# Performance work log

Hardware: AMD Instinct MI355X
Metric: run time of the kernel (lower is better)

## Reference

```python
import jax, jax.numpy as jnp
import numpy as np


def setup_inputs() -> dict:
    key = jax.random.key(0)
    k1, k2 = jax.random.split(key, 2)
    N, C, H, W, G = 64, 256, 56, 56, 32
    x = jax.random.normal(k1, (N, C, H, W), dtype=jnp.float32)
    # fc: Linear(batch_size*2 -> group)
    fc_w = jax.random.normal(k2, (G, 2 * N), dtype=jnp.float32) * 0.05
    fc_b = jnp.zeros((G,), dtype=jnp.float32)
    # affine params (1, C, 1, 1), init ones/zeros as in the module
    weight = jnp.ones((1, C, 1, 1), dtype=jnp.float32)
    bias = jnp.zeros((1, C, 1, 1), dtype=jnp.float32)
    return {"x": x, "fc_w": fc_w, "fc_b": fc_b, "weight": weight, "bias": bias, "group": G}


def reference(x, fc_w, fc_b, weight, bias, group):
    eps = 1e-5
    N, C, H, W = x.shape
    hw = H * W
    # --- routing features: per-channel mean/var over (N is kept, reduce HW) ---
    # torch: x_ = x.transpose(0,1).view(C,N,HW); mean/var(-1) with unbiased var (ddof=1)
    mean_cn = jnp.mean(x, axis=(2, 3)).T           # [C, N]
    var_cn = jnp.var(x, axis=(2, 3), ddof=1).T     # [C, N]
    s = jnp.concatenate([mean_cn, var_cn], axis=1)  # [C, 2N]
    probs = jax.nn.softmax(s @ fc_w.T + fc_b, axis=1)  # [C, G]
    g = jnp.argmax(probs, axis=1)                  # [C] channel -> group
    onehot = jax.nn.one_hot(g, group, dtype=x.dtype)  # [C, G]
    # --- per-(sample, group) mean/var via segment reduce expressed as GEMM ---
    s1 = jnp.sum(x, axis=(2, 3))        # [N, C]
    s2 = jnp.sum(x * x, axis=(2, 3))    # [N, C]
    S1 = s1 @ onehot                    # [N, G]
    S2 = s2 @ onehot                    # [N, G]
    cnt = jnp.sum(onehot, axis=0) * hw  # [G] elements per (n, g)
    mean_g = S1 / jnp.maximum(cnt, 1.0)                          # [N, G]
    # unbiased variance (torch .var default): (sum_sq - n*mean^2)/(n-1)
    var_g = (S2 - S1 * mean_g) / jnp.maximum(cnt - 1.0, 1.0)     # [N, G]
    # empty groups are skipped in the original; no channel maps to them, so
    # the guarded denominators only prevent NaNs and never affect outputs.
    mean_c = mean_g[:, g]  # [N, C] gather per-channel stats
    var_c = var_g[:, g]    # [N, C]
    xn = (x - mean_c[:, :, None, None]) * jax.lax.rsqrt(var_c + eps)[:, :, None, None]
    return xn * weight + bias
```

## Files before the change

kernel.cpp:

```cpp
#include <hip/hip_runtime.h>

constexpr int N_  = 64;
constexpr int C_  = 256;
constexpr int HW_ = 56 * 56;
constexpr int G_  = 32;
constexpr int NC_ = N_ * C_;
constexpr float EPS_ = 1e-5f;

typedef float f32x4 __attribute__((ext_vector_type(4)));

__global__ __launch_bounds__(256) void k_sums(const float* __restrict__ x,
                                              float* __restrict__ s1,
                                              float* __restrict__ s2) {
    const int wave = threadIdx.x >> 6;
    const int lane = threadIdx.x & 63;
    const int nc = blockIdx.x * 4 + wave;
    const f32x4* xp = reinterpret_cast<const f32x4*>(x + (size_t)nc * HW_);
    f32x4 v[12];
    #pragma unroll
    for (int k = 0; k < 12; ++k) v[k] = xp[lane + k * 64];
    f32x4 vt;
    const bool tail = lane < 16;
    if (tail) vt = xp[768 + lane];
    float a = 0.f, b = 0.f;
    #pragma unroll
    for (int k = 0; k < 12; ++k) {
        a += (v[k].x + v[k].y) + (v[k].z + v[k].w);
        b += (v[k].x * v[k].x + v[k].y * v[k].y) + (v[k].z * v[k].z + v[k].w * v[k].w);
    }
    if (tail) {
        a += (vt.x + vt.y) + (vt.z + vt.w);
        b += (vt.x * vt.x + vt.y * vt.y) + (vt.z * vt.z + vt.w * vt.w);
    }
    #pragma unroll
    for (int off = 32; off; off >>= 1) {
        a += __shfl_down(a, off, 64);
        b += __shfl_down(b, off, 64);
    }
    if (lane == 0) { s1[nc] = a; s2[nc] = b; }
}

__global__ __launch_bounds__(64) void k_logits(const float* __restrict__ s1,
                                               const float* __restrict__ s2,
                                               const float* __restrict__ fc_w,
                                               const float* __restrict__ fc_b,
                                               int* __restrict__ gidx) {
    const int c = blockIdx.x;
    const int t = threadIdx.x;
    const int g = t & 31, half = t >> 5;
    const float inv_hw  = 1.f / (float)HW_;
    const float inv_hw1 = 1.f / (float)(HW_ - 1);
    const float* wg = fc_w + g * (2 * N_);
    float acc = half ? 0.f : fc_b[g];
    const int n0 = half * 32;
    #pragma unroll 8
    for (int n = n0; n < n0 + 32; ++n) {
        const float v1 = s1[n * C_ + c];
        const float v2 = s2[n * C_ + c];
        const float m  = v1 * inv_hw;
        const float vr = (v2 - v1 * m) * inv_hw1;
        acc += m * wg[n] + vr * wg[N_ + n];
    }
    acc += __shfl_down(acc, 32, 64);
    __shared__ float lg[G_];
    if (half == 0) lg[g] = acc;
    __syncthreads();
    if (t == 0) {
        float best = lg[0];
        int bi = 0;
        for (int g2 = 1; g2 < G_; ++g2) {
            const float v = lg[g2];
            if (v > best) { best = v; bi = g2; }
        }
        gidx[c] = bi;
    }
}

__global__ __launch_bounds__(256) void k_group(const float* __restrict__ s1,
                                               const float* __restrict__ s2,
                                               const int* __restrict__ gidx,
                                               const float* __restrict__ weight,
                                               const float* __restrict__ bias,
                                               float* __restrict__ scale,
                                               float* __restrict__ shift) {
    const int n = blockIdx.x;
    const int c = threadIdx.x;
    __shared__ float r1[C_], r2[C_];
    __shared__ int   gi[C_];
    __shared__ float mg[G_], ig[G_];
    r1[c] = s1[n * C_ + c];
    r2[c] = s2[n * C_ + c];
    gi[c] = gidx[c];
    __syncthreads();
    if (c < G_) {
        float A = 0.f, B = 0.f;
        int k = 0;
        for (int cc = 0; cc < C_; ++cc) {
            if (gi[cc] == c) { A += r1[cc]; B += r2[cc]; ++k; }
        }
        const float cf = (float)k * (float)HW_;
        const float m  = A / fmaxf(cf, 1.f);
        const float vr = (B - A * m) / fmaxf(cf - 1.f, 1.f);
        mg[c] = m;
        ig[c] = rsqrtf(vr + EPS_);
    }
    __syncthreads();
    const int g = gi[c];
    const float sc = ig[g] * weight[c];
    scale[n * C_ + c] = sc;
    shift[n * C_ + c] = bias[c] - mg[g] * sc;
}

__global__ __launch_bounds__(256) void k_norm(const float* __restrict__ x,
                                              const float* __restrict__ scale,
                                              const float* __restrict__ shift,
                                              float* __restrict__ out) {
    const int wave = threadIdx.x >> 6;
    const int lane = threadIdx.x & 63;
    const int nc = blockIdx.x * 4 + wave;
    const float sc = scale[nc];
    const float sh = shift[nc];
    const f32x4* xp = reinterpret_cast<const f32x4*>(x + (size_t)nc * HW_);
    f32x4* op = reinterpret_cast<f32x4*>(out + (size_t)nc * HW_);
    f32x4 v[12];
    #pragma unroll
    for (int k = 0; k < 12; ++k) v[k] = xp[lane + k * 64];
    f32x4 vt;
    const bool tail = lane < 16;
    if (tail) vt = xp[768 + lane];
    #pragma unroll
    for (int k = 0; k < 12; ++k) {
        v[k] = v[k] * sc + sh;
        __builtin_nontemporal_store(v[k], op + lane + k * 64);
    }
    if (tail) {
        vt = vt * sc + sh;
        __builtin_nontemporal_store(vt, op + 768 + lane);
    }
}

extern "C" void kernel_launch(void* const* d_in, const int* in_sizes, int n_in,
                              void* d_out, int out_size, void* d_ws, size_t ws_size,
                              hipStream_t stream) {
    const float* x      = (const float*)d_in[0];
    const float* fc_w   = (const float*)d_in[1];
    const float* fc_b   = (const float*)d_in[2];
    const float* weight = (const float*)d_in[3];
    const float* bias   = (const float*)d_in[4];
    float* out = (float*)d_out;

    float* ws    = (float*)d_ws;
    float* s1    = ws;
    float* s2    = ws + NC_;
    float* scale = ws + 2 * NC_;
    float* shift = ws + 3 * NC_;
    int*   gidx  = (int*)(ws + 4 * NC_);

    k_sums  <<<NC_ / 4, 256, 0, stream>>>(x, s1, s2);
    k_logits<<<C_,       64, 0, stream>>>(s1, s2, fc_w, fc_b, gidx);
    k_group <<<N_,      256, 0, stream>>>(s1, s2, gidx, weight, bias, scale, shift);
    k_norm  <<<NC_ / 4, 256, 0, stream>>>(x, scale, shift, out);
}
```

Before: 120.6 us.

## Fuse four kernels into one cooperative kernel keeping part of x in registers

Replaces the four-kernel pipeline (sums, logits, group stats, normalize) with a single cooperative kernel of 256 blocks that uses grid-wide syncs between phases. Each wave holds the first 5 of 12 vector chunks of its 8 channel slices in registers across the syncs, so the normalize pass reloads only the rest of x instead of all of it. This cuts launch overhead and some re-reading of x from memory. The cost is two grid barriers, heavy register pressure that may limit occupancy or spill, and only 256 blocks to hide memory latency.

```diff
diff --git a/kernel.cpp b/kernel.cpp
--- a/kernel.cpp
+++ b/kernel.cpp
@@ -1,141 +1,168 @@
 #include <hip/hip_runtime.h>
+#include <hip/hip_cooperative_groups.h>
+
+namespace cg = cooperative_groups;
 
 constexpr int N_  = 64;
 constexpr int C_  = 256;
 constexpr int HW_ = 56 * 56;
+constexpr int NV_ = HW_ / 4;
 constexpr int G_  = 32;
 constexpr int NC_ = N_ * C_;
 constexpr float EPS_ = 1e-5f;
 
 typedef float f32x4 __attribute__((ext_vector_type(4)));
 
-__global__ __launch_bounds__(256) void k_sums(const float* __restrict__ x,
-                                              float* __restrict__ s1,
-                                              float* __restrict__ s2) {
-    const int wave = threadIdx.x >> 6;
-    const int lane = threadIdx.x & 63;
-    const int nc = blockIdx.x * 4 + wave;
-    const f32x4* xp = reinterpret_cast<const f32x4*>(x + (size_t)nc * HW_);
-    f32x4 v[12];
+__global__ __launch_bounds__(512, 2) void k_fused(
+    const float* __restrict__ x,
+    const float* __restrict__ fc_w,
+    const float* __restrict__ fc_b,
+    const float* __restrict__ weight,
+    const float* __restrict__ bias,
+    float* __restrict__ out,
+    float* __restrict__ s1,
+    float* __restrict__ s2,
+    int*   __restrict__ gidxg)
+{
+    const int b    = blockIdx.x;
+    const int t    = threadIdx.x;
+    const int w    = t >> 6;
+    const int lane = t & 63;
+    const int n    = b >> 2;
+    const int c0   = (b & 3) * 64;
+    const int slice0 = b * 64 + w * 8;
+
+    __shared__ float r1s[C_], r2s[C_];
+    __shared__ int   gidxL[C_];
+    __shared__ float mgs[G_], igs[G_];
+    __shared__ float scs[64], shs[64];
+
+    f32x4 keep[8][5];
     #pragma unroll
-    for (int k = 0; k < 12; ++k) v[k] = xp[lane + k * 64];
-    f32x4 vt;
-    const bool tail = lane < 16;
-    if (tail) vt = xp[768 + lane];
-    float a = 0.f, b = 0.f;
-    #pragma unroll
-    for (int k = 0; k < 12; ++k) {
-        a += (v[k].x + v[k].y) + (v[k].z + v[k].w);
-        b += (v[k].x * v[k].x + v[k].y * v[k].y) + (v[k].z * v[k].z + v[k].w * v[k].w);
+    for (int s = 0; s < 8; ++s) {
+        const int nc = slice0 + s;
+        const f32x4* xp = reinterpret_cast<const f32x4*>(x) + (size_t)nc * NV_;
+        #pragma unroll
+        for (int k = 0; k < 5; ++k) keep[s][k] = xp[lane + k * 64];
+        f32x4 v5  = xp[lane + 320];
+        f32x4 v6  = xp[lane + 384];
+        f32x4 v7  = xp[lane + 448];
+        f32x4 v8  = xp[lane + 512];
+        f32x4 v9  = xp[lane + 576];
+        f32x4 v10 = xp[lane + 640];
+        f32x4 v11 = xp[lane + 704];
+        const bool tail = lane < 16;
+        f32x4 vt;
+        if (tail) vt = xp[768 + lane];
+        float a = 0.f, q = 0.f;
+        #pragma unroll
+        for (int k = 0; k < 5; ++k) {
+            f32x4 v = keep[s][k];
+            a += (v.x + v.y) + (v.z + v.w);
+            q += (v.x * v.x + v.y * v.y) + (v.z * v.z + v.w * v.w);
+        }
+        a += (v5.x + v5.y) + (v5.z + v5.w);   q += (v5.x*v5.x + v5.y*v5.y) + (v5.z*v5.z + v5.w*v5.w);
+        a += (v6.x + v6.y) + (v6.z + v6.w);   q += (v6.x*v6.x + v6.y*v6.y) + (v6.z*v6.z + v6.w*v6.w);
+        a += (v7.x + v7.y) + (v7.z + v7.w);   q += (v7.x*v7.x + v7.y*v7.y) + (v7.z*v7.z + v7.w*v7.w);
+        a += (v8.x + v8.y) + (v8.z + v8.w);   q += (v8.x*v8.x + v8.y*v8.y) + (v8.z*v8.z + v8.w*v8.w);
+        a += (v9.x + v9.y) + (v9.z + v9.w);   q += (v9.x*v9.x + v9.y*v9.y) + (v9.z*v9.z + v9.w*v9.w);
+        a += (v10.x + v10.y) + (v10.z + v10.w); q += (v10.x*v10.x + v10.y*v10.y) + (v10.z*v10.z + v10.w*v10.w);
+        a += (v11.x + v11.y) + (v11.z + v11.w); q += (v11.x*v11.x + v11.y*v11.y) + (v11.z*v11.z + v11.w*v11.w);
+        if (tail) {
+            a += (vt.x + vt.y) + (vt.z + vt.w);
+            q += (vt.x*vt.x + vt.y*vt.y) + (vt.z*vt.z + vt.w*vt.w);
+        }
+        #pragma unroll
+        for (int off = 32; off; off >>= 1) {
+            a += __shfl_down(a, off, 64);
+            q += __shfl_down(q, off, 64);
+        }
+        if (lane == 0) {
+            __hip_atomic_store(&s1[nc], a, __ATOMIC_RELAXED, __HIP_MEMORY_SCOPE_AGENT);
+            __hip_atomic_store(&s2[nc], q, __ATOMIC_RELAXED, __HIP_MEMORY_SCOPE_AGENT);
+        }
     }
-    if (tail) {
-        a += (vt.x + vt.y) + (vt.z + vt.w);
-        b += (vt.x * vt.x + vt.y * vt.y) + (vt.z * vt.z + vt.w * vt.w);
+
+    __threadfence();
+    cg::this_grid().sync();
+
+    if (t < 64) {
+        const int c = b;
+        const int g = lane & 31, half = lane >> 5;
+        const float inv_hw  = 1.f / (float)HW_;
+        const float inv_hw1 = 1.f / (float)(HW_ - 1);
+        const float* wg = fc_w + g * (2 * N_);
+        float acc = half ? 0.f : fc_b[g];
+        const int n0 = half * 32;
+        #pragma unroll
+        for (int nn = n0; nn < n0 + 32; ++nn) {
+            const float a1 = __hip_atomic_load(&s1[nn * C_ + c], __ATOMIC_RELAXED, __HIP_MEMORY_SCOPE_AGENT);
+            const float a2 = __hip_atomic_load(&s2[nn * C_ + c], __ATOMIC_RELAXED, __HIP_MEMORY_SCOPE_AGENT);
+            const float m  = a1 * inv_hw;
+            const float vr = (a2 - a1 * m) * inv_hw1;
+            acc += m * wg[nn] + vr * wg[N_ + nn];
+        }
+        acc += __shfl_down(acc, 32, 64);
+        float bv = acc; int bi = g;
+        #pragma unroll
+        for (int off = 16; off; off >>= 1) {
+            float ov = __shfl_down(bv, off, 32);
+            int   oi = __shfl_down(bi, off, 32);
+            if (ov > bv || (ov == bv && oi < bi)) { bv = ov; bi = oi; }
+        }
+        if (lane == 0)
+            __hip_atomic_store(&gidxg[c], bi, __ATOMIC_RELAXED, __HIP_MEMORY_SCOPE_AGENT);
     }
-    #pragma unroll
-    for (int off = 32; off; off >>= 1) {
-        a += __shfl_down(a, off, 64);
-        b += __shfl_down(b, off, 64);
+
+    __threadfence();
+    cg::this_grid().sync();
+
+    if (t < 256) {
+        r1s[t]   = __hip_atomic_load(&s1[n * C_ + t], __ATOMIC_RELAXED, __HIP_MEMORY_SCOPE_AGENT);
+        gidxL[t] = __hip_atomic_load(&gidxg[t],       __ATOMIC_RELAXED, __HIP_MEMORY_SCOPE_AGENT);
+    } else {
+        r2s[t - 256] = __hip_atomic_load(&s2[n * C_ + (t - 256)], __ATOMIC_RELAXED, __HIP_MEMORY_SCOPE_AGENT);
     }
-    if (lane == 0) { s1[nc] = a; s2[nc] = b; }
-}
-
-__global__ __launch_bounds__(64) void k_logits(const float* __restrict__ s1,
-                                               const float* __restrict__ s2,
-                                               const float* __restrict__ fc_w,
-                                               const float* __restrict__ fc_b,
-                                               int* __restrict__ gidx) {
-    const int c = blockIdx.x;
-    const int t = threadIdx.x;
-    const int g = t & 31, half = t >> 5;
-    const float inv_hw  = 1.f / (float)HW_;
-    const float inv_hw1 = 1.f / (float)(HW_ - 1);
-    const float* wg = fc_w + g * (2 * N_);
-    float acc = half ? 0.f : fc_b[g];
-    const int n0 = half * 32;
-    #pragma unroll 8
-    for (int n = n0; n < n0 + 32; ++n) {
-        const float v1 = s1[n * C_ + c];
-        const float v2 = s2[n * C_ + c];
-        const float m  = v1 * inv_hw;
-        const float vr = (v2 - v1 * m) * inv_hw1;
-        acc += m * wg[n] + vr * wg[N_ + n];
-    }
-    acc += __shfl_down(acc, 32, 64);
-    __shared__ float lg[G_];
-    if (half == 0) lg[g] = acc;
     __syncthreads();
-    if (t == 0) {
-        float best = lg[0];
-        int bi = 0;
-        for (int g2 = 1; g2 < G_; ++g2) {
-            const float v = lg[g2];
-            if (v > best) { best = v; bi = g2; }
-        }
-        gidx[c] = bi;
-    }
-}
-
-__global__ __launch_bounds__(256) void k_group(const float* __restrict__ s1,
-                                               const float* __restrict__ s2,
-                                               const int* __restrict__ gidx,
-                                               const float* __restrict__ weight,
-                                               const float* __restrict__ bias,
-                                               float* __restrict__ scale,
-                                               float* __restrict__ shift) {
-    const int n = blockIdx.x;
-    const int c = threadIdx.x;
-    __shared__ float r1[C_], r2[C_];
-    __shared__ int   gi[C_];
-    __shared__ float mg[G_], ig[G_];
-    r1[c] = s1[n * C_ + c];
-    r2[c] = s2[n * C_ + c];
-    gi[c] = gidx[c];
-    __syncthreads();
-    if (c < G_) {
-        float A = 0.f, B = 0.f;
-        int k = 0;
-        for (int cc = 0; cc < C_; ++cc) {
-            if (gi[cc] == c) { A += r1[cc]; B += r2[cc]; ++k; }
-        }
+    if (t < G_) {
+        float A = 0.f, B = 0.f; int k = 0;
+        for (int cc = 0; cc < C_; ++cc)
+            if (gidxL[cc] == t) { A += r1s[cc]; B += r2s[cc]; ++k; }
         const float cf = (float)k * (float)HW_;
         const float m  = A / fmaxf(cf, 1.f);
         const float vr = (B - A * m) / fmaxf(cf - 1.f, 1.f);
-        mg[c] = m;
-        ig[c] = rsqrtf(vr + EPS_);
+        mgs[t] = m;
+        igs[t] = rsqrtf(vr + EPS_);
     }
     __syncthreads();
-    const int g = gi[c];
-    const float sc = ig[g] * weight[c];
-    scale[n * C_ + c] = sc;
-    shift[n * C_ + c] = bias[c] - mg[g] * sc;
-}
+    if (t < 64) {
+        const int c = c0 + t;
+        const int g = gidxL[c];
+        const float sc = igs[g] * weight[c];
+        scs[t] = sc;
+        shs[t] = bias[c] - mgs[g] * sc;
+    }
+    __syncthreads();
 
-__global__ __launch_bounds__(256) void k_norm(const float* __restrict__ x,
-                                              const float* __restrict__ scale,
-                                              const float* __restrict__ shift,
-                                              float* __restrict__ out) {
-    const int wave = threadIdx.x >> 6;
-    const int lane = threadIdx.x & 63;
-    const int nc = blockIdx.x * 4 + wave;
-    const float sc = scale[nc];
-    const float sh = shift[nc];
-    const f32x4* xp = reinterpret_cast<const f32x4*>(x + (size_t)nc * HW_);
-    f32x4* op = reinterpret_cast<f32x4*>(out + (size_t)nc * HW_);
-    f32x4 v[12];
     #pragma unroll
-    for (int k = 0; k < 12; ++k) v[k] = xp[lane + k * 64];
-    f32x4 vt;
-    const bool tail = lane < 16;
-    if (tail) vt = xp[768 + lane];
-    #pragma unroll
-    for (int k = 0; k < 12; ++k) {
-        v[k] = v[k] * sc + sh;
-        __builtin_nontemporal_store(v[k], op + lane + k * 64);
-    }
-    if (tail) {
-        vt = vt * sc + sh;
-        __builtin_nontemporal_store(vt, op + 768 + lane);
+    for (int s = 0; s < 8; ++s) {
+        const int nc = slice0 + s;
+        const float sc = scs[w * 8 + s];
+        const float sh = shs[w * 8 + s];
+        const f32x4* xp = reinterpret_cast<const f32x4*>(x)   + (size_t)nc * NV_;
+        f32x4*       op = reinterpret_cast<f32x4*>(out)       + (size_t)nc * NV_;
+        #pragma unroll
+        for (int k = 0; k < 5; ++k)
+            __builtin_nontemporal_store(keep[s][k] * sc + sh, op + lane + k * 64);
+        #pragma unroll
+        for (int k = 5; k < 12; ++k) {
+            f32x4 v = xp[lane + k * 64];
+            __builtin_nontemporal_store(v * sc + sh, op + lane + k * 64);
+        }
+        if (lane < 16) {
+            f32x4 v = xp[768 + lane];
+            __builtin_nontemporal_store(v * sc + sh, op + 768 + lane);
+        }
     }
 }
 
@@ -147,17 +174,14 @@
     const float* fc_b   = (const float*)d_in[2];
     const float* weight = (const float*)d_in[3];
     const float* bias   = (const float*)d_in[4];
-    float* out = (float*)d_out;
+    float* outp = (float*)d_out;
 
-    float* ws    = (float*)d_ws;
-    float* s1    = ws;
-    float* s2    = ws + NC_;
-    float* scale = ws + 2 * NC_;
-    float* shift = ws + 3 * NC_;
-    int*   gidx  = (int*)(ws + 4 * NC_);
+    float* ws = (float*)d_ws;
+    float* s1 = ws;
+    float* s2 = ws + NC_;
+    int*   gidxg = (int*)(ws + 2 * NC_);
 
-    k_sums  <<<NC_ / 4, 256, 0, stream>>>(x, s1, s2);
-    k_logits<<<C_,       64, 0, stream>>>(s1, s2, fc_w, fc_b, gidx);
-    k_group <<<N_,      256, 0, stream>>>(s1, s2, gidx, weight, bias, scale, shift);
-    k_norm  <<<NC_ / 4, 256, 0, stream>>>(x, scale, shift, out);
+    void* args[] = { (void*)&x, (void*)&fc_w, (void*)&fc_b, (void*)&weight, (void*)&bias,
+                     (void*)&outp, (void*)&s1, (void*)&s2, (void*)&gidxg };
+    hipLaunchCooperativeKernel((void*)k_fused, dim3(256), dim3(512), args, 0, stream);
 }
```

Result: slower. 289.3 us (+139.8%).

## Fuse four-stage pipeline into one cooperative persistent kernel with grid syncs

Applied to the files above, without the earlier changes.

Replaces the four separate launches (sums, logits, group stats, normalize) with a single cooperative persistent kernel that separates the phases with grid-wide syncs, falling back to the old launches if occupancy is too low. The aim is to remove launch gaps and tail effects between the small middle kernels. In exchange it adds three grid barriers, limits the grid to 1024 blocks, and leaves the x reads in the normalize phase still going through memory, since 205 MB of x cannot stay cached. The logits argmax now uses a wave shuffle reduction instead of a serial loop.

```diff
diff --git a/kernel.cpp b/kernel.cpp
--- a/kernel.cpp
+++ b/kernel.cpp
@@ -1,13 +1,151 @@
 #include <hip/hip_runtime.h>
+#include <hip/hip_cooperative_groups.h>
+
+namespace cg = cooperative_groups;
 
 constexpr int N_  = 64;
 constexpr int C_  = 256;
 constexpr int HW_ = 56 * 56;
+constexpr int NV_ = HW_ / 4;
 constexpr int G_  = 32;
 constexpr int NC_ = N_ * C_;
 constexpr float EPS_ = 1e-5f;
 
 typedef float f32x4 __attribute__((ext_vector_type(4)));
+
+__global__ __launch_bounds__(256, 4) void k_fused(
+    const float* __restrict__ x,
+    const float* __restrict__ fc_w,
+    const float* __restrict__ fc_b,
+    const float* __restrict__ weight,
+    const float* __restrict__ bias,
+    float* __restrict__ out,
+    float* __restrict__ s1,
+    float* __restrict__ s2,
+    float* __restrict__ scale,
+    float* __restrict__ shift,
+    int*   __restrict__ gidxg)
+{
+    const int t    = threadIdx.x;
+    const int w    = t >> 6;
+    const int lane = t & 63;
+    const int nwaves = gridDim.x * 4;
+
+    __shared__ float r1s[C_], r2s[C_];
+    __shared__ int   gidxL[C_];
+    __shared__ float mgs[G_], igs[G_];
+
+    for (int nc = blockIdx.x * 4 + w; nc < NC_; nc += nwaves) {
+        const f32x4* xp = reinterpret_cast<const f32x4*>(x) + (size_t)nc * NV_;
+        f32x4 v[12];
+        #pragma unroll
+        for (int k = 0; k < 12; ++k) v[k] = xp[lane + k * 64];
+        const bool tail = lane < 16;
+        f32x4 vt;
+        if (tail) vt = xp[768 + lane];
+        float a = 0.f, q = 0.f;
+        #pragma unroll
+        for (int k = 0; k < 12; ++k) {
+            a += (v[k].x + v[k].y) + (v[k].z + v[k].w);
+            q += (v[k].x * v[k].x + v[k].y * v[k].y) + (v[k].z * v[k].z + v[k].w * v[k].w);
+        }
+        if (tail) {
+            a += (vt.x + vt.y) + (vt.z + vt.w);
+            q += (vt.x * vt.x + vt.y * vt.y) + (vt.z * vt.z + vt.w * vt.w);
+        }
+        #pragma unroll
+        for (int off = 32; off; off >>= 1) {
+            a += __shfl_down(a, off, 64);
+            q += __shfl_down(q, off, 64);
+        }
+        if (lane == 0) {
+            __hip_atomic_store(&s1[nc], a, __ATOMIC_RELAXED, __HIP_MEMORY_SCOPE_AGENT);
+            __hip_atomic_store(&s2[nc], q, __ATOMIC_RELAXED, __HIP_MEMORY_SCOPE_AGENT);
+        }
+    }
+
+    __threadfence();
+    cg::this_grid().sync();
+
+    for (int c = blockIdx.x; c < C_; c += gridDim.x) {
+        if (t < 64) {
+            const int g = lane & 31, half = lane >> 5;
+            const float inv_hw  = 1.f / (float)HW_;
+            const float inv_hw1 = 1.f / (float)(HW_ - 1);
+            const float* wg = fc_w + g * (2 * N_);
+            float acc = half ? 0.f : fc_b[g];
+            const int n0 = half * 32;
+            #pragma unroll
+            for (int nn = n0; nn < n0 + 32; ++nn) {
+                const float a1 = __hip_atomic_load(&s1[nn * C_ + c], __ATOMIC_RELAXED, __HIP_MEMORY_SCOPE_AGENT);
+                const float a2 = __hip_atomic_load(&s2[nn * C_ + c], __ATOMIC_RELAXED, __HIP_MEMORY_SCOPE_AGENT);
+                const float m  = a1 * inv_hw;
+                const float vr = (a2 - a1 * m) * inv_hw1;
+                acc += m * wg[nn] + vr * wg[N_ + nn];
+            }
+            acc += __shfl_down(acc, 32, 64);
+            float bv = acc; int bi = g;
+            #pragma unroll
+            for (int off = 16; off; off >>= 1) {
+                float ov = __shfl_down(bv, off, 32);
+                int   oi = __shfl_down(bi, off, 32);
+                if (ov > bv || (ov == bv && oi < bi)) { bv = ov; bi = oi; }
+            }
+            if (lane == 0)
+                __hip_atomic_store(&gidxg[c], bi, __ATOMIC_RELAXED, __HIP_MEMORY_SCOPE_AGENT);
+        }
+    }
+
+    __threadfence();
+    cg::this_grid().sync();
+
+    for (int n = blockIdx.x; n < N_; n += gridDim.x) {
+        __syncthreads();
+        r1s[t]   = __hip_atomic_load(&s1[n * C_ + t], __ATOMIC_RELAXED, __HIP_MEMORY_SCOPE_AGENT);
+        r2s[t]   = __hip_atomic_load(&s2[n * C_ + t], __ATOMIC_RELAXED, __HIP_MEMORY_SCOPE_AGENT);
+        gidxL[t] = __hip_atomic_load(&gidxg[t],       __ATOMIC_RELAXED, __HIP_MEMORY_SCOPE_AGENT);
+        __syncthreads();
+        if (t < G_) {
+            float A = 0.f, B = 0.f; int k = 0;
+            for (int cc = 0; cc < C_; ++cc)
+                if (gidxL[cc] == t) { A += r1s[cc]; B += r2s[cc]; ++k; }
+            const float cf = (float)k * (float)HW_;
+            const float m  = A / fmaxf(cf, 1.f);
+            const float vr = (B - A * m) / fmaxf(cf - 1.f, 1.f);
+            mgs[t] = m;
+            igs[t] = rsqrtf(vr + EPS_);
+        }
+        __syncthreads();
+        {
+            const int c = t;
+            const int g = gidxL[c];
+            const float sc = igs[g] * weight[c];
+            __hip_atomic_store(&scale[n * C_ + c], sc, __ATOMIC_RELAXED, __HIP_MEMORY_SCOPE_AGENT);
+            __hip_atomic_store(&shift[n * C_ + c], bias[c] - mgs[g] * sc, __ATOMIC_RELAXED, __HIP_MEMORY_SCOPE_AGENT);
+        }
+    }
+
+    __threadfence();
+    cg::this_grid().sync();
+
+    for (int nc = blockIdx.x * 4 + w; nc < NC_; nc += nwaves) {
+        const float sc = __hip_atomic_load(&scale[nc], __ATOMIC_RELAXED, __HIP_MEMORY_SCOPE_AGENT);
+        const float sh = __hip_atomic_load(&shift[nc], __ATOMIC_RELAXED, __HIP_MEMORY_SCOPE_AGENT);
+        const f32x4* xp = reinterpret_cast<const f32x4*>(x)  + (size_t)nc * NV_;
+        f32x4*       op = reinterpret_cast<f32x4*>(out)      + (size_t)nc * NV_;
+        f32x4 v[12];
+        #pragma unroll
+        for (int k = 0; k < 12; ++k) v[k] = xp[lane + k * 64];
+        const bool tail = lane < 16;
+        f32x4 vt;
+        if (tail) vt = xp[768 + lane];
+        #pragma unroll
+        for (int k = 0; k < 12; ++k)
+            __builtin_nontemporal_store(v[k] * sc + sh, op + lane + k * 64);
+        if (tail)
+            __builtin_nontemporal_store(vt * sc + sh, op + 768 + lane);
+    }
+}
 
 __global__ __launch_bounds__(256) void k_sums(const float* __restrict__ x,
                                               float* __restrict__ s1,
@@ -129,14 +267,10 @@
     const bool tail = lane < 16;
     if (tail) vt = xp[768 + lane];
     #pragma unroll
-    for (int k = 0; k < 12; ++k) {
-        v[k] = v[k] * sc + sh;
-        __builtin_nontemporal_store(v[k], op + lane + k * 64);
-    }
-    if (tail) {
-        vt = vt * sc + sh;
-        __builtin_nontemporal_store(vt, op + 768 + lane);
-    }
+    for (int k = 0; k < 12; ++k)
+        __builtin_nontemporal_store(v[k] * sc + sh, op + lane + k * 64);
+    if (tail)
+        __builtin_nontemporal_store(vt * sc + sh, op + 768 + lane);
 }
 
 extern "C" void kernel_launch(void* const* d_in, const int* in_sizes, int n_in,
@@ -147,17 +281,32 @@
     const float* fc_b   = (const float*)d_in[2];
     const float* weight = (const float*)d_in[3];
     const float* bias   = (const float*)d_in[4];
-    float* out = (float*)d_out;
+    float* outp = (float*)d_out;
 
     float* ws    = (float*)d_ws;
     float* s1    = ws;
     float* s2    = ws + NC_;
     float* scale = ws + 2 * NC_;
     float* shift = ws + 3 * NC_;
-    int*   gidx  = (int*)(ws + 4 * NC_);
-
-    k_sums  <<<NC_ / 4, 256, 0, stream>>>(x, s1, s2);
-    k_logits<<<C_,       64, 0, stream>>>(s1, s2, fc_w, fc_b, gidx);
-    k_group <<<N_,      256, 0, stream>>>(s1, s2, gidx, weight, bias, scale, shift);
-    k_norm  <<<NC_ / 4, 256, 0, stream>>>(x, scale, shift, out);
-}
+    int*   gidxg = (int*)(ws + 4 * NC_);
+
+    int bpc = 0;
+    hipError_t oe = hipOccupancyMaxActiveBlocksPerMultiprocessor(&bpc, k_fused, 256, 0);
+    int grid = 0;
+    if (oe == hipSuccess && bpc > 0) {
+        grid = bpc * 256;
+        if (grid > 1024) grid = 1024;
+    }
+
+    if (grid >= 64) {
+        void* args[] = { (void*)&x, (void*)&fc_w, (void*)&fc_b, (void*)&weight, (void*)&bias,
+                         (void*)&outp, (void*)&s1, (void*)&s2, (void*)&scale, (void*)&shift,
+                         (void*)&gidxg };
+        hipLaunchCooperativeKernel((void*)k_fused, dim3(grid), dim3(256), args, 0, stream);
+    } else {
+        k_sums  <<<NC_ / 4, 256, 0, stream>>>(x, s1, s2);
+        k_logits<<<C_,       64, 0, stream>>>(s1, s2, fc_w, fc_b, gidxg);
+        k_group <<<N_,      256, 0, stream>>>(s1, s2, gidxg, weight, bias, scale, shift);
+        k_norm  <<<NC_ / 4, 256, 0, stream>>>(x, scale, shift, outp);
+    }
+}
```

Result: slower. 406.1 us (+236.7%).
